# Kernel optimization log

Hardware: AMD Instinct MI355X
Metric: run time of the kernel (lower is better)

The kernel has to match this reference:

```python
import jax, jax.numpy as jnp
import numpy as np

B, N, D_IN, D_HID, D_OUT = 4096, 64, 128, 128, 128


def setup_inputs() -> dict:
    key = jax.random.key(0)
    k1, k2, k3, k4, k5, k6 = jax.random.split(key, 6)
    inp = jax.random.normal(k1, (B, D_IN), dtype=jnp.float32)
    neigh = jax.random.normal(k2, (B, N, D_IN), dtype=jnp.float32)
    # zero out some neighbors so the mask path is exercised
    drop = jax.random.bernoulli(k3, 0.2, (B, N))
    neigh = jnp.where(drop[:, :, None], 0.0, neigh)
    W_mlp = jax.random.normal(k4, (D_HID, D_IN), dtype=jnp.float32) * (1.0 / np.sqrt(D_IN))
    b_mlp = jnp.zeros((D_HID,), dtype=jnp.float32)
    W_comb = jax.random.normal(k5, (2 * D_OUT, D_IN + D_HID), dtype=jnp.float32) * (1.0 / np.sqrt(D_IN + D_HID))
    b_comb = jax.random.normal(k6, (2 * D_OUT,), dtype=jnp.float32) * 0.01
    return {"input": inp, "neighbor_inputs": neigh, "W_mlp": W_mlp, "b_mlp": b_mlp,
            "W_comb": W_comb, "b_comb": b_comb}


def reference(input, neighbor_inputs, W_mlp, b_mlp, W_comb, b_comb):
    # mask: neighbors whose features sum to exactly 0 (padding)  [B, N, 1]
    mask = (jnp.sum(neighbor_inputs, axis=-1) == 0.0)[:, :, None]
    # per-neighbor MLP + ReLU: [B, N, D_HID]
    h = jax.nn.relu(jnp.einsum('bnd,hd->bnh', neighbor_inputs, W_mlp) + b_mlp)
    h = jnp.where(mask, 0.0, h)
    # max-pool over neighbor dim -> [B, D_HID]
    pooled = jnp.max(h, axis=1)
    # combine: concat + linear + ReLU -> [B, 2*D_OUT]
    combined = jnp.concatenate([input, pooled], axis=-1)
    out = jax.nn.relu(combined @ W_comb.T + b_comb)
    return out
```

## Files before the change

### kernel.cpp

```cpp
#include <hip/hip_runtime.h>
#include <hip/hip_bf16.h>

typedef __attribute__((ext_vector_type(4))) float f32x4;
typedef __attribute__((ext_vector_type(8))) short bf16x8;

#define N_NEI 64
#define D_IN  128
#define D_HID 128

union BF8 { bf16x8 v; __hip_bfloat162 h[4]; unsigned u[4]; };

__device__ __forceinline__ bf16x8 pack8(const float4& a, const float4& b) {
  BF8 r;
  r.h[0] = __float22bfloat162_rn(float2{a.x, a.y});
  r.h[1] = __float22bfloat162_rn(float2{a.z, a.w});
  r.h[2] = __float22bfloat162_rn(float2{b.x, b.y});
  r.h[3] = __float22bfloat162_rn(float2{b.z, b.w});
  return r.v;
}

__global__ __launch_bounds__(256, 2)
void k1_pool(const float* __restrict__ neigh, const float* __restrict__ Wmlp,
             const float* __restrict__ bmlp, unsigned short* __restrict__ pooled) {
  __shared__ unsigned short Wl[D_HID * D_IN];
  __shared__ float pscr[4][D_HID];

  const int tid = threadIdx.x;
  const int l = tid & 63;
  const int w = tid >> 6;
  const int lr = l & 15;
  const int lg = l >> 4;

  const int b = blockIdx.x * 4 + w;
  const float* rowbase = neigh + (size_t)b * N_NEI * D_IN;

  float4 pf[16];
  {
    const float* ra = rowbase + (size_t)lr * D_IN + lg * 8;
    const float* rb = rowbase + (size_t)(16 + lr) * D_IN + lg * 8;
    #pragma unroll
    for (int ks = 0; ks < 4; ++ks) {
      pf[2 * ks]      = *(const float4*)(ra + ks * 32);
      pf[2 * ks + 1]  = *(const float4*)(ra + ks * 32 + 4);
      pf[8 + 2 * ks]  = *(const float4*)(rb + ks * 32);
      pf[9 + 2 * ks]  = *(const float4*)(rb + ks * 32 + 4);
    }
  }

  const float4* W4 = (const float4*)Wmlp;
  #pragma unroll
  for (int it = 0; it < 8; ++it) {
    int f8 = it * 256 + tid;
    int j  = f8 >> 4;
    int d0 = (f8 & 15) * 8;
    float4 a = W4[f8 * 2];
    float4 bb = W4[f8 * 2 + 1];
    int byte = j * 256 + ((d0 * 2) ^ ((j & 7) << 4));
    *(bf16x8*)((char*)Wl + byte) = pack8(a, bb);
  }

  float bml[8];
  #pragma unroll
  for (int t = 0; t < 8; ++t) bml[t] = bmlp[t * 16 + lr];

  __syncthreads();

  float pmax[8];
  #pragma unroll
  for (int t = 0; t < 8; ++t) pmax[t] = 0.f;

  #pragma unroll 1
  for (int it = 0; it < 2; ++it) {
    bf16x8 afA[4], afB[4];
    float rsA = 0.f, rsB = 0.f;
    #pragma unroll
    for (int ks = 0; ks < 4; ++ks) {
      float4 a0 = pf[2 * ks],     a1 = pf[2 * ks + 1];
      float4 b0 = pf[8 + 2 * ks], b1 = pf[9 + 2 * ks];
      rsA += a0.x + a0.y + a0.z + a0.w + a1.x + a1.y + a1.z + a1.w;
      rsB += b0.x + b0.y + b0.z + b0.w + b1.x + b1.y + b1.z + b1.w;
      afA[ks] = pack8(a0, a1);
      afB[ks] = pack8(b0, b1);
    }

    if (it == 0) {
      const float* ra = rowbase + (size_t)(32 + lr) * D_IN + lg * 8;
      const float* rb = rowbase + (size_t)(48 + lr) * D_IN + lg * 8;
      #pragma unroll
      for (int ks = 0; ks < 4; ++ks) {
        pf[2 * ks]      = *(const float4*)(ra + ks * 32);
        pf[2 * ks + 1]  = *(const float4*)(ra + ks * 32 + 4);
        pf[8 + 2 * ks]  = *(const float4*)(rb + ks * 32);
        pf[9 + 2 * ks]  = *(const float4*)(rb + ks * 32 + 4);
      }
    }

    rsA += __shfl_xor(rsA, 16); rsA += __shfl_xor(rsA, 32);
    rsB += __shfl_xor(rsB, 16); rsB += __shfl_xor(rsB, 32);
    unsigned maskA = (unsigned)(__ballot(rsA == 0.0f) & 0xFFFFull);
    unsigned maskB = (unsigned)(__ballot(rsB == 0.0f) & 0xFFFFull);

    #pragma unroll 1
    for (int p = 0; p < 2; ++p) {
      f32x4 accA[4], accB[4];
      #pragma unroll
      for (int tt = 0; tt < 4; ++tt) {
        accA[tt] = (f32x4){0.f, 0.f, 0.f, 0.f};
        accB[tt] = (f32x4){0.f, 0.f, 0.f, 0.f};
      }

      #pragma unroll
      for (int tt = 0; tt < 4; ++tt) {
        #pragma unroll
        for (int ks = 0; ks < 4; ++ks) {
          int jr = (p * 4 + tt) * 16 + lr;
          int d0 = ks * 32 + lg * 8;
          bf16x8 bf = *(const bf16x8*)((const char*)Wl + jr * 256 + ((d0 * 2) ^ ((jr & 7) << 4)));
          accA[tt] = __builtin_amdgcn_mfma_f32_16x16x32_bf16(afA[ks], bf, accA[tt], 0, 0, 0);
          accB[tt] = __builtin_amdgcn_mfma_f32_16x16x32_bf16(afB[ks], bf, accB[tt], 0, 0, 0);
        }
      }

      #pragma unroll
      for (int tt = 0; tt < 4; ++tt) {
        #pragma unroll
        for (int r = 0; r < 4; ++r) {
          int row = lg * 4 + r;
          float vA = fmaxf(accA[tt][r] + bml[p * 4 + tt], 0.f);
          float vB = fmaxf(accB[tt][r] + bml[p * 4 + tt], 0.f);
          if ((maskA >> row) & 1u) vA = 0.f;
          if ((maskB >> row) & 1u) vB = 0.f;
          pmax[p * 4 + tt] = fmaxf(pmax[p * 4 + tt], fmaxf(vA, vB));
        }
      }
    }
  }

  #pragma unroll
  for (int t = 0; t < 8; ++t) {
    pmax[t] = fmaxf(pmax[t], __shfl_xor(pmax[t], 16));
    pmax[t] = fmaxf(pmax[t], __shfl_xor(pmax[t], 32));
  }

  if (l < 16) {
    #pragma unroll
    for (int t = 0; t < 8; ++t) pscr[w][t * 16 + l] = pmax[t];
  }
  __syncthreads();
  float2 pv = *(const float2*)&pscr[w][2 * l];
  __hip_bfloat162 h2 = __float22bfloat162_rn(pv);
  ((unsigned*)(pooled + (size_t)b * D_HID))[l] = *(unsigned*)&h2;
}

__global__ __launch_bounds__(256, 2)
void k2_comb(const float* __restrict__ inp, const unsigned short* __restrict__ pooled,
             const float* __restrict__ Wcomb, const float* __restrict__ bcomb,
             float* __restrict__ out) {
  __shared__ unsigned short Wl[64 * 256];

  const int tid = threadIdx.x;
  const int l = tid & 63;
  const int w = tid >> 6;
  const int mchunk = blockIdx.x >> 2;
  const int colq   = blockIdx.x & 3;
  const int lr = l & 15;
  const int lg = l >> 4;

  const int row = mchunk * 64 + w * 16 + lr;

  float4 a0[4], a1[4];
  #pragma unroll
  for (int ks = 0; ks < 4; ++ks) {
    const float* p = inp + (size_t)row * 128 + ks * 32 + lg * 8;
    a0[ks] = *(const float4*)p;
    a1[ks] = *(const float4*)(p + 4);
  }
  bf16x8 af[8];
  #pragma unroll
  for (int ks = 4; ks < 8; ++ks) {
    af[ks] = *(const bf16x8*)(pooled + (size_t)row * 128 + (ks - 4) * 32 + lg * 8);
  }

  const float4* W4 = (const float4*)Wcomb;
  #pragma unroll
  for (int it = 0; it < 8; ++it) {
    int c  = it * 256 + tid;
    int jr = c >> 5;
    int d0 = (c & 31) * 8;
    int gidx = ((colq * 64 + jr) * 256 + d0) >> 2;
    float4 a = W4[gidx];
    float4 bb = W4[gidx + 1];
    int byte = jr * 512 + ((d0 * 2) ^ ((jr & 7) << 4));
    *(bf16x8*)((char*)Wl + byte) = pack8(a, bb);
  }

  float bcl[4];
  #pragma unroll
  for (int t = 0; t < 4; ++t) bcl[t] = bcomb[colq * 64 + t * 16 + lr];

  #pragma unroll
  for (int ks = 0; ks < 4; ++ks) af[ks] = pack8(a0[ks], a1[ks]);

  __syncthreads();

  f32x4 acc[4];
  #pragma unroll
  for (int t = 0; t < 4; ++t) acc[t] = (f32x4){0.f, 0.f, 0.f, 0.f};
  #pragma unroll
  for (int t = 0; t < 4; ++t) {
    #pragma unroll
    for (int ks = 0; ks < 8; ++ks) {
      int jr = t * 16 + lr;
      int d0 = ks * 32 + lg * 8;
      bf16x8 bf = *(const bf16x8*)((const char*)Wl + jr * 512 + ((d0 * 2) ^ ((jr & 7) << 4)));
      acc[t] = __builtin_amdgcn_mfma_f32_16x16x32_bf16(af[ks], bf, acc[t], 0, 0, 0);
    }
  }

  #pragma unroll
  for (int t = 0; t < 4; ++t) {
    #pragma unroll
    for (int r = 0; r < 4; ++r) {
      int ro = mchunk * 64 + w * 16 + lg * 4 + r;
      int co = colq * 64 + t * 16 + lr;
      float v = acc[t][r] + bcl[t];
      out[(size_t)ro * 256 + co] = fmaxf(v, 0.f);
    }
  }
}

extern "C" void kernel_launch(void* const* d_in, const int* in_sizes, int n_in,
                              void* d_out, int out_size, void* d_ws, size_t ws_size,
                              hipStream_t stream) {
  const float* inp   = (const float*)d_in[0];
  const float* neigh = (const float*)d_in[1];
  const float* Wmlp  = (const float*)d_in[2];
  const float* bmlp  = (const float*)d_in[3];
  const float* Wcomb = (const float*)d_in[4];
  const float* bcomb = (const float*)d_in[5];
  float* out = (float*)d_out;
  unsigned short* pooled = (unsigned short*)d_ws;

  k1_pool<<<1024, 256, 0, stream>>>(neigh, Wmlp, bmlp, pooled);
  k2_comb<<<256, 256, 0, stream>>>(inp, pooled, Wcomb, bcomb, out);
}
```

Measured before the change: 36.75 us.

## Preconvert weights to swizzled bf16 once and DMA them into LDS

A small pre-kernel converts W_mlp and W_comb to bf16 in the swizzled LDS layout once per call, writing them to workspace. The pool and combine kernels then copy the ready-made tiles straight into shared memory with global_load_lds instead of each block loading fp32 and converting. The combine kernel also splits its output columns into eight slices instead of four, doubling its grid and halving per-block LDS. The cost is an extra kernel launch and a dependency between kernels.

```diff
diff --git a/kernel.cpp b/kernel.cpp
--- a/kernel.cpp
+++ b/kernel.cpp
@@ -19,8 +19,29 @@
   return r.v;
 }
 
+__global__ __launch_bounds__(256)
+void conv_w(const float* __restrict__ Wmlp, const float* __restrict__ Wcomb,
+            unsigned short* __restrict__ wmlp_bf, unsigned short* __restrict__ wcomb_bf) {
+  int t = blockIdx.x * 256 + threadIdx.x;
+  if (t < 2048) {
+    int j = t >> 4, d0 = (t & 15) * 8;
+    const float* p = Wmlp + j * 128 + d0;
+    float4 a = *(const float4*)p, b = *(const float4*)(p + 4);
+    int byte = j * 256 + ((d0 * 2) ^ ((j & 7) << 4));
+    *(bf16x8*)((char*)wmlp_bf + byte) = pack8(a, b);
+  } else if (t < 2048 + 8192) {
+    int c = t - 2048;
+    int jg = c >> 5, d0 = (c & 31) * 8;
+    const float* p = Wcomb + jg * 256 + d0;
+    float4 a = *(const float4*)p, b = *(const float4*)(p + 4);
+    int s = jg >> 5, jr = jg & 31;
+    int byte = s * 16384 + jr * 512 + ((d0 * 2) ^ ((jr & 7) << 4));
+    *(bf16x8*)((char*)wcomb_bf + byte) = pack8(a, b);
+  }
+}
+
 __global__ __launch_bounds__(256, 2)
-void k1_pool(const float* __restrict__ neigh, const float* __restrict__ Wmlp,
+void k1_pool(const float* __restrict__ neigh, const unsigned short* __restrict__ wmlp_bf,
              const float* __restrict__ bmlp, unsigned short* __restrict__ pooled) {
   __shared__ unsigned short Wl[D_HID * D_IN];
   __shared__ float pscr[4][D_HID];
@@ -47,16 +68,16 @@
     }
   }
 
-  const float4* W4 = (const float4*)Wmlp;
-  #pragma unroll
-  for (int it = 0; it < 8; ++it) {
-    int f8 = it * 256 + tid;
-    int j  = f8 >> 4;
-    int d0 = (f8 & 15) * 8;
-    float4 a = W4[f8 * 2];
-    float4 bb = W4[f8 * 2 + 1];
-    int byte = j * 256 + ((d0 * 2) ^ ((j & 7) << 4));
-    *(bf16x8*)((char*)Wl + byte) = pack8(a, bb);
+  {
+    const char* wsrc = (const char*)wmlp_bf;
+    #pragma unroll
+    for (int i = 0; i < 8; ++i) {
+      int off = (i * 4 + w) * 1024;
+      __builtin_amdgcn_global_load_lds(
+        (const __attribute__((address_space(1))) unsigned int*)(wsrc + off + l * 16),
+        (__attribute__((address_space(3))) unsigned int*)((char*)Wl + off),
+        16, 0, 0);
+    }
   }
 
   float bml[8];
@@ -154,15 +175,15 @@
 
 __global__ __launch_bounds__(256, 2)
 void k2_comb(const float* __restrict__ inp, const unsigned short* __restrict__ pooled,
-             const float* __restrict__ Wcomb, const float* __restrict__ bcomb,
+             const unsigned short* __restrict__ wcomb_bf, const float* __restrict__ bcomb,
              float* __restrict__ out) {
-  __shared__ unsigned short Wl[64 * 256];
+  __shared__ unsigned short Wl[32 * 256];
 
   const int tid = threadIdx.x;
   const int l = tid & 63;
   const int w = tid >> 6;
-  const int mchunk = blockIdx.x >> 2;
-  const int colq   = blockIdx.x & 3;
+  const int mchunk = blockIdx.x >> 3;
+  const int c8     = blockIdx.x & 7;
   const int lr = l & 15;
   const int lg = l >> 4;
 
@@ -181,33 +202,32 @@
     af[ks] = *(const bf16x8*)(pooled + (size_t)row * 128 + (ks - 4) * 32 + lg * 8);
   }
 
-  const float4* W4 = (const float4*)Wcomb;
-  #pragma unroll
-  for (int it = 0; it < 8; ++it) {
-    int c  = it * 256 + tid;
-    int jr = c >> 5;
-    int d0 = (c & 31) * 8;
-    int gidx = ((colq * 64 + jr) * 256 + d0) >> 2;
-    float4 a = W4[gidx];
-    float4 bb = W4[gidx + 1];
-    int byte = jr * 512 + ((d0 * 2) ^ ((jr & 7) << 4));
-    *(bf16x8*)((char*)Wl + byte) = pack8(a, bb);
-  }
-
-  float bcl[4];
-  #pragma unroll
-  for (int t = 0; t < 4; ++t) bcl[t] = bcomb[colq * 64 + t * 16 + lr];
+  {
+    const char* wsrc = (const char*)wcomb_bf + c8 * 16384;
+    #pragma unroll
+    for (int i = 0; i < 4; ++i) {
+      int off = (i * 4 + w) * 1024;
+      __builtin_amdgcn_global_load_lds(
+        (const __attribute__((address_space(1))) unsigned int*)(wsrc + off + l * 16),
+        (__attribute__((address_space(3))) unsigned int*)((char*)Wl + off),
+        16, 0, 0);
+    }
+  }
+
+  float bcl[2];
+  #pragma unroll
+  for (int t = 0; t < 2; ++t) bcl[t] = bcomb[c8 * 32 + t * 16 + lr];
 
   #pragma unroll
   for (int ks = 0; ks < 4; ++ks) af[ks] = pack8(a0[ks], a1[ks]);
 
   __syncthreads();
 
-  f32x4 acc[4];
-  #pragma unroll
-  for (int t = 0; t < 4; ++t) acc[t] = (f32x4){0.f, 0.f, 0.f, 0.f};
-  #pragma unroll
-  for (int t = 0; t < 4; ++t) {
+  f32x4 acc[2];
+  #pragma unroll
+  for (int t = 0; t < 2; ++t) acc[t] = (f32x4){0.f, 0.f, 0.f, 0.f};
+  #pragma unroll
+  for (int t = 0; t < 2; ++t) {
     #pragma unroll
     for (int ks = 0; ks < 8; ++ks) {
       int jr = t * 16 + lr;
@@ -218,11 +238,11 @@
   }
 
   #pragma unroll
-  for (int t = 0; t < 4; ++t) {
+  for (int t = 0; t < 2; ++t) {
     #pragma unroll
     for (int r = 0; r < 4; ++r) {
       int ro = mchunk * 64 + w * 16 + lg * 4 + r;
-      int co = colq * 64 + t * 16 + lr;
+      int co = c8 * 32 + t * 16 + lr;
       float v = acc[t][r] + bcl[t];
       out[(size_t)ro * 256 + co] = fmaxf(v, 0.f);
     }
@@ -239,8 +259,12 @@
   const float* Wcomb = (const float*)d_in[4];
   const float* bcomb = (const float*)d_in[5];
   float* out = (float*)d_out;
-  unsigned short* pooled = (unsigned short*)d_ws;
-
-  k1_pool<<<1024, 256, 0, stream>>>(neigh, Wmlp, bmlp, pooled);
-  k2_comb<<<256, 256, 0, stream>>>(inp, pooled, Wcomb, bcomb, out);
-}
+
+  unsigned short* pooled   = (unsigned short*)d_ws;
+  unsigned short* wmlp_bf  = (unsigned short*)((char*)d_ws + (1 << 20));
+  unsigned short* wcomb_bf = (unsigned short*)((char*)d_ws + (1 << 20) + 32768);
+
+  conv_w<<<40, 256, 0, stream>>>(Wmlp, Wcomb, wmlp_bf, wcomb_bf);
+  k1_pool<<<1024, 256, 0, stream>>>(neigh, wmlp_bf, bmlp, pooled);
+  k2_comb<<<512, 256, 0, stream>>>(inp, pooled, wcomb_bf, bcomb, out);
+}
```

Result: slower. 42.65 us (+16.0%).
